# Performance work log

Hardware: AMD Instinct MI355X
Metric: run time of the kernel (lower is better)

## Reference

```python
import jax, jax.numpy as jnp
import numpy as np

N_HIDDEN = 2048
N_HEADS = 64
EXPAND = 2
D_STATE = 128
D_CONV = 4
CHUNK = 128
DT_MIN = 0.001
DT_MAX = 0.1
INNER = EXPAND * N_HIDDEN            # 4096
HEAD_DIM = INNER // N_HEADS          # 64
CONV_DIM = INNER + 2 * D_STATE       # 4352
D_IN_PROJ = 2 * INNER + 2 * D_STATE + N_HEADS  # 8512
EPS = 1e-6


def setup_inputs() -> dict:
    key = jax.random.key(0)
    ks = jax.random.split(key, 10)
    B, L = 2, 2048
    s = lambda fan_in: 1.0 / np.sqrt(fan_in)
    return {
        "x": jax.random.normal(ks[0], (B, L, N_HIDDEN), jnp.float32),
        "W_in": jax.random.normal(ks[1], (N_HIDDEN, D_IN_PROJ), jnp.float32) * s(N_HIDDEN),
        "b_in": jnp.zeros((D_IN_PROJ,), jnp.float32),
        "conv_w": jax.random.normal(ks[2], (D_CONV, 1, CONV_DIM), jnp.float32) * s(D_CONV),
        "conv_b": jnp.zeros((CONV_DIM,), jnp.float32),
        "A_log": jnp.log(jnp.arange(1, N_HEADS + 1, dtype=jnp.float32)),
        "dt_bias": jax.random.normal(ks[3], (N_HEADS,), jnp.float32) * 0.1,
        "D_param": jnp.ones((N_HEADS,), jnp.float32),
        "norm_w": jnp.ones((INNER,), jnp.float32),
        "W_out": jax.random.normal(ks[4], (INNER, N_HIDDEN), jnp.float32) * s(INNER),
        "b_out": jnp.zeros((N_HIDDEN,), jnp.float32),
    }


def _segsum(x):
    t = x.shape[-1]
    cs = jnp.cumsum(x, axis=-1)
    seg = cs[..., :, None] - cs[..., None, :]
    mask = jnp.tril(jnp.ones((t, t), dtype=bool))
    return jnp.where(mask, seg, -jnp.inf)


def _ssd(x, dt, a, b_mat, c_mat, d, dt_bias):
    # x: (B,L,H,P)  dt: (B,L,H)  a: (H,)  b_mat/c_mat: (B,L,H,N)  d: (H,)
    bsz, seq, h, p = x.shape
    dt = jnp.clip(jax.nn.softplus(dt + dt_bias), DT_MIN, DT_MAX)
    d_res = d.reshape(1, 1, h, 1) * x
    x_disc = x * dt[..., None]
    a_disc = a * dt                                   # (B,L,H)
    ch = lambda t_: t_.reshape(bsz, seq // CHUNK, CHUNK, *t_.shape[2:])
    x_blk, b_blk, c_blk = ch(x_disc), ch(b_mat), ch(c_mat)
    a_blk = jnp.transpose(ch(a_disc), (0, 3, 1, 2))   # (B,H,C,Lc)
    a_cum = jnp.cumsum(a_blk, axis=-1)
    l_mat = jnp.exp(_segsum(a_blk))                   # (B,H,C,Lc,Lc)
    y_diag = jnp.einsum("bclhn,bcshn,bhcls,bcshp->bclhp", c_blk, b_blk, l_mat, x_blk)
    decay_states = jnp.exp(a_cum[..., -1:] - a_cum)
    states = jnp.einsum("bclhn,bhcl,bclhp->bchpn", b_blk, decay_states, x_blk)
    states = jnp.concatenate([jnp.zeros_like(states[:, :1]), states], axis=1)
    a_end = jnp.pad(a_cum[..., -1], ((0, 0), (0, 0), (1, 0)))
    decay_chunk = jnp.exp(_segsum(a_end))
    new_states = jnp.einsum("bhzc,bchpn->bzhpn", decay_chunk, states)
    states = new_states[:, :-1]
    y_off = jnp.einsum("bclhn,bchpn,bhcl->bclhp", c_blk, states, jnp.exp(a_cum))
    y = (y_diag + y_off).reshape(bsz, seq, h, p)
    return y + d_res


def reference(x, W_in, b_in, conv_w, conv_b, A_log, dt_bias, D_param, norm_w, W_out, b_out):
    B, L, _ = x.shape
    zxbcdt = x @ W_in + b_in
    z = zxbcdt[..., :INNER]
    xBC = zxbcdt[..., INNER:INNER + CONV_DIM]
    dt = zxbcdt[..., -N_HEADS:]
    # causal depthwise conv1d + silu
    xp = jnp.pad(xBC, ((0, 0), (D_CONV - 1, 0), (0, 0)))
    xBC = jax.lax.conv_general_dilated(
        xp, conv_w, window_strides=(1,), padding="VALID",
        dimension_numbers=("NWC", "WIO", "NWC"), feature_group_count=CONV_DIM,
    ) + conv_b
    xBC = jax.nn.silu(xBC)
    x_ssm = xBC[..., :INNER].reshape(B, L, N_HEADS, HEAD_DIM)
    b_mat = jnp.broadcast_to(xBC[..., INNER:INNER + D_STATE][:, :, None, :], (B, L, N_HEADS, D_STATE))
    c_mat = jnp.broadcast_to(xBC[..., INNER + D_STATE:][:, :, None, :], (B, L, N_HEADS, D_STATE))
    a = -jnp.exp(A_log)
    y = _ssd(x_ssm, dt, a, b_mat, c_mat, D_param, dt_bias)
    y = y.reshape(B, L, INNER)
    # gated RMSNorm
    y = y * jax.nn.silu(z)
    y = y * jax.lax.rsqrt(jnp.mean(y * y, axis=-1, keepdims=True) + EPS) * norm_w
    return y @ W_out + b_out
```

## Files before the change

### kernel.cpp

```cpp
#include <hip/hip_runtime.h>
#include <hip/hip_bf16.h>
#include <cstdint>

typedef __bf16 bf16x8 __attribute__((ext_vector_type(8)));
typedef __bf16 bf16x4 __attribute__((ext_vector_type(4)));
typedef float  f4     __attribute__((ext_vector_type(4)));

constexpr int BATCH   = 2;
constexpr int LSEQ    = 2048;
constexpr int NH      = 2048;
constexpr int INNER   = 4096;
constexpr int DSTATE  = 128;
constexpr int CONVD   = 4352;
constexpr int HEADS   = 64;
constexpr int HDIM    = 64;
constexpr int NPROJ   = 8512;
constexpr int NPROJ_P = 8576;
constexpr int NC      = 16;
constexpr int CH      = 128;
constexpr int ROWS    = BATCH * LSEQ;
constexpr int NBC     = BATCH * NC;

__device__ __forceinline__ f4 f4zero() { f4 v; v.x=0.f; v.y=0.f; v.z=0.f; v.w=0.f; return v; }

__device__ __forceinline__ void gload16(const __bf16* g, __bf16* l) {
    __builtin_amdgcn_global_load_lds((const __attribute__((address_space(1))) void*)g,
                                     (__attribute__((address_space(3))) void*)l, 16, 0, 0);
}

__global__ __launch_bounds__(256) void k_cast_bf16(const float* __restrict__ in,
                                                   __bf16* __restrict__ out, int n4) {
    int i = blockIdx.x * 256 + threadIdx.x;
    if (i >= n4) return;
    f4 v = ((const f4*)in)[i];
    bf16x4 o;
    o[0] = (__bf16)v.x; o[1] = (__bf16)v.y; o[2] = (__bf16)v.z; o[3] = (__bf16)v.w;
    ((bf16x4*)out)[i] = o;
}

__global__ __launch_bounds__(256) void k_transpose_cast(const float* __restrict__ in,
                                                        __bf16* __restrict__ out,
                                                        int R, int C, int Cp) {
    __shared__ float tile[32][33];
    int bn = blockIdx.x * 32, bk = blockIdx.y * 32;
    int tx = threadIdx.x & 31, ty = threadIdx.x >> 5;
#pragma unroll
    for (int i = 0; i < 4; ++i) {
        int k = bk + ty + i * 8, n = bn + tx;
        tile[ty + i * 8][tx] = (k < R && n < C) ? in[(size_t)k * C + n] : 0.f;
    }
    __syncthreads();
#pragma unroll
    for (int i = 0; i < 4; ++i) {
        int n = bn + ty + i * 8, k = bk + tx;
        if (n < Cp && k < R) out[(size_t)n * R + k] = (__bf16)tile[tx][ty + i * 8];
    }
}

__global__ __launch_bounds__(256) void k_gemm1(const __bf16* __restrict__ A,
                                               const __bf16* __restrict__ Bt,
                                               const float* __restrict__ bias,
                                               __bf16* __restrict__ zf,
                                               __bf16* __restrict__ xbcpre,
                                               float* __restrict__ dtraw) {
    constexpr int K = NH;
    __shared__ __bf16 As[128 * 32];
    __shared__ __bf16 Bs[128 * 32];
    int tid = threadIdx.x;
    int lane = tid & 63, wave = tid >> 6;
    int wr = wave >> 1, wc = wave & 1;
    int mBase = blockIdx.y * 128, nBase = blockIdx.x * 128;
    int srow = lane >> 2, scol = (lane & 3) * 8;
    const __bf16* ga0 = A  + (size_t)(mBase + wave * 16 + srow) * K + scol;
    const __bf16* ga1 = ga0 + (size_t)64 * K;
    const __bf16* gb0 = Bt + (size_t)(nBase + wave * 16 + srow) * K + scol;
    const __bf16* gb1 = gb0 + (size_t)64 * K;
    __bf16* la0 = As + (wave * 16) * 32;
    __bf16* la1 = As + (64 + wave * 16) * 32;
    __bf16* lb0 = Bs + (wave * 16) * 32;
    __bf16* lb1 = Bs + (64 + wave * 16) * 32;
    f4 acc[4][4];
#pragma unroll
    for (int i = 0; i < 4; ++i)
#pragma unroll
        for (int j = 0; j < 4; ++j) acc[i][j] = f4zero();
    int kq = (lane >> 4) * 8, rl = lane & 15;
    for (int k0 = 0; k0 < K; k0 += 32) {
        __syncthreads();
        gload16(ga0 + k0, la0);
        gload16(ga1 + k0, la1);
        gload16(gb0 + k0, lb0);
        gload16(gb1 + k0, lb1);
        __syncthreads();
        bf16x8 af[4], bf[4];
#pragma unroll
        for (int i = 0; i < 4; ++i) {
            af[i] = *(const bf16x8*)&As[(wr * 64 + i * 16 + rl) * 32 + kq];
            bf[i] = *(const bf16x8*)&Bs[(wc * 64 + i * 16 + rl) * 32 + kq];
        }
#pragma unroll
        for (int mi = 0; mi < 4; ++mi)
#pragma unroll
            for (int ni = 0; ni < 4; ++ni)
                acc[mi][ni] = __builtin_amdgcn_mfma_f32_16x16x32_bf16(af[mi], bf[ni], acc[mi][ni], 0, 0, 0);
    }
    int rq = lane >> 4, cl = lane & 15;
#pragma unroll
    for (int ni = 0; ni < 4; ++ni) {
        int col0 = nBase + wc * 64 + ni * 16;
        int col = col0 + cl;
        if (col0 >= NPROJ) continue;
        float bv = bias[col];
#pragma unroll
        for (int mi = 0; mi < 4; ++mi) {
#pragma unroll
            for (int j = 0; j < 4; ++j) {
                int row = mBase + wr * 64 + mi * 16 + rq * 4 + j;
                float v = acc[mi][ni][j] + bv;
                if (col0 < INNER) {
                    zf[(size_t)row * INNER + col] = (__bf16)v;
                } else if (col0 < INNER + CONVD) {
                    xbcpre[(size_t)row * CONVD + (col - INNER)] = (__bf16)v;
                } else {
                    dtraw[(size_t)row * HEADS + (col - INNER - CONVD)] = v;
                }
            }
        }
    }
}

__global__ __launch_bounds__(256) void k_gemm_bf16(const __bf16* __restrict__ A,
                                                   const __bf16* __restrict__ Bt,
                                                   const float* __restrict__ bias,
                                                   float* __restrict__ C, int N, int K) {
    __shared__ __bf16 As[128 * 32];
    __shared__ __bf16 Bs[128 * 32];
    int tid = threadIdx.x;
    int lane = tid & 63, wave = tid >> 6;
    int wr = wave >> 1, wc = wave & 1;
    int mBase = blockIdx.y * 128, nBase = blockIdx.x * 128;
    int srow = lane >> 2, scol = (lane & 3) * 8;
    const __bf16* ga0 = A  + (size_t)(mBase + wave * 16 + srow) * K + scol;
    const __bf16* ga1 = ga0 + (size_t)64 * K;
    const __bf16* gb0 = Bt + (size_t)(nBase + wave * 16 + srow) * K + scol;
    const __bf16* gb1 = gb0 + (size_t)64 * K;
    __bf16* la0 = As + (wave * 16) * 32;
    __bf16* la1 = As + (64 + wave * 16) * 32;
    __bf16* lb0 = Bs + (wave * 16) * 32;
    __bf16* lb1 = Bs + (64 + wave * 16) * 32;
    f4 acc[4][4];
#pragma unroll
    for (int i = 0; i < 4; ++i)
#pragma unroll
        for (int j = 0; j < 4; ++j) acc[i][j] = f4zero();
    int kq = (lane >> 4) * 8, rl = lane & 15;
    for (int k0 = 0; k0 < K; k0 += 32) {
        __syncthreads();
        gload16(ga0 + k0, la0);
        gload16(ga1 + k0, la1);
        gload16(gb0 + k0, lb0);
        gload16(gb1 + k0, lb1);
        __syncthreads();
        bf16x8 af[4], bf[4];
#pragma unroll
        for (int i = 0; i < 4; ++i) {
            af[i] = *(const bf16x8*)&As[(wr * 64 + i * 16 + rl) * 32 + kq];
            bf[i] = *(const bf16x8*)&Bs[(wc * 64 + i * 16 + rl) * 32 + kq];
        }
#pragma unroll
        for (int mi = 0; mi < 4; ++mi)
#pragma unroll
            for (int ni = 0; ni < 4; ++ni)
                acc[mi][ni] = __builtin_amdgcn_mfma_f32_16x16x32_bf16(af[mi], bf[ni], acc[mi][ni], 0, 0, 0);
    }
    int rq = lane >> 4, cl = lane & 15;
#pragma unroll
    for (int ni = 0; ni < 4; ++ni) {
        int col = nBase + wc * 64 + ni * 16 + cl;
        float bv = bias[col];
#pragma unroll
        for (int mi = 0; mi < 4; ++mi)
#pragma unroll
            for (int j = 0; j < 4; ++j) {
                int row = mBase + wr * 64 + mi * 16 + rq * 4 + j;
                C[(size_t)row * N + col] = acc[mi][ni][j] + bv;
            }
    }
}

__global__ __launch_bounds__(256) void k_conv_silu(const __bf16* __restrict__ xbcpre,
                                                   const float* __restrict__ conv_w,
                                                   const float* __restrict__ conv_b,
                                                   __bf16* __restrict__ xbc) {
    int idx = blockIdx.x * 256 + threadIdx.x;
    int c8 = idx % (CONVD / 8);
    int bl = idx / (CONVD / 8);
    int l = bl & (LSEQ - 1);
    int c0 = c8 * 8;
    float acc[8];
    const f4* cb4 = (const f4*)(conv_b + c0);
    f4 b0 = cb4[0], b1 = cb4[1];
#pragma unroll
    for (int k = 0; k < 4; ++k) { acc[k] = b0[k]; acc[k + 4] = b1[k]; }
#pragma unroll
    for (int j = 0; j < 4; ++j) {
        int l2 = l + j - 3;
        if (l2 < 0) continue;
        bf16x8 xv = *(const bf16x8*)(xbcpre + (size_t)(bl + j - 3) * CONVD + c0);
        const f4* w4 = (const f4*)(conv_w + j * CONVD + c0);
        f4 w0 = w4[0], w1 = w4[1];
#pragma unroll
        for (int k = 0; k < 4; ++k) {
            acc[k]     += w0[k] * (float)xv[k];
            acc[k + 4] += w1[k] * (float)xv[k + 4];
        }
    }
    bf16x8 o;
#pragma unroll
    for (int k = 0; k < 8; ++k) {
        float a = acc[k];
        o[k] = (__bf16)(a / (1.f + expf(-a)));
    }
    *(bf16x8*)(xbc + (size_t)bl * CONVD + c0) = o;
}

__global__ __launch_bounds__(256) void k_dt(const float* __restrict__ dtraw,
                                            const float* __restrict__ dt_bias,
                                            float* __restrict__ dtp_t) {
    int idx = blockIdx.x * 256 + threadIdx.x;
    int h = idx & 63;
    int bl = idx >> 6;
    int b = bl >> 11, l = bl & (LSEQ - 1);
    float raw = dtraw[idx] + dt_bias[h];
    float sp = raw > 20.f ? raw : log1pf(expf(raw));
    dtp_t[((size_t)(b * HEADS + h)) * LSEQ + l] = fminf(fmaxf(sp, 0.001f), 0.1f);
}

__global__ __launch_bounds__(256) void k_transpose_bc(const __bf16* __restrict__ xbc,
                                                      __bf16* __restrict__ xT,
                                                      __bf16* __restrict__ BtG) {
    int bid = blockIdx.x;
    int ct = bid % 66;
    int rt = (bid / 66) & 1;
    int bc = bid / 132;
    __shared__ float T[64][65];
    int t = threadIdx.x;
    int lr0 = t >> 3, cg = t & 7;
#pragma unroll
    for (int it = 0; it < 2; ++it) {
        int lr = lr0 + it * 32;
        bf16x8 v = *(const bf16x8*)(xbc + (size_t)(bc * CH + rt * 64 + lr) * CONVD + ct * 64 + cg * 8);
#pragma unroll
        for (int j = 0; j < 8; ++j) T[lr][cg * 8 + j] = (float)v[j];
    }
    __syncthreads();
#pragma unroll
    for (int it = 0; it < 2; ++it) {
        int cl = lr0 + it * 32;
        int c = ct * 64 + cl;
        bf16x8 o;
#pragma unroll
        for (int j = 0; j < 8; ++j) o[j] = (__bf16)T[cg * 8 + j][cl];
        __bf16* dst = (c < INNER)
            ? xT  + ((size_t)bc * INNER + c) * CH + rt * 64 + cg * 8
            : BtG + ((size_t)bc * DSTATE + (c - INNER)) * CH + rt * 64 + cg * 8;
        *(bf16x8*)dst = o;
    }
}

__global__ __launch_bounds__(256) void k_cb(const __bf16* __restrict__ xbc,
                                            float* __restrict__ cbT) {
    int bid = blockIdx.x;
    int lg = bid & 7, bc = bid >> 3;
    int tid = threadIdx.x;
    int e0 = lg * 2048 + tid * 8;
    int l = e0 >> 7;
    int s0 = e0 & 127;
    const __bf16* Crow = xbc + (size_t)(bc * CH + l) * CONVD + INNER + DSTATE;
    const __bf16* B0   = xbc + (size_t)(bc * CH + s0) * CONVD + INNER;
    float acc[8];
#pragma unroll
    for (int j = 0; j < 8; ++j) acc[j] = 0.f;
    for (int n8 = 0; n8 < 16; ++n8) {
        bf16x8 cv = *(const bf16x8*)(Crow + n8 * 8);
        float cf[8];
#pragma unroll
        for (int k = 0; k < 8; ++k) cf[k] = (float)cv[k];
#pragma unroll
        for (int j = 0; j < 8; ++j) {
            bf16x8 bv = *(const bf16x8*)(B0 + (size_t)j * CONVD + n8 * 8);
#pragma unroll
            for (int k = 0; k < 8; ++k) acc[j] += cf[k] * (float)bv[k];
        }
    }
    float* dst = cbT + ((size_t)bc << 14) + (l << 7) + s0;
#pragma unroll
    for (int j = 0; j < 8; ++j) dst[j] = (s0 + j <= l) ? acc[j] : 0.f;
}

__global__ __launch_bounds__(256) void k_states(const __bf16* __restrict__ xT,
                                                const __bf16* __restrict__ BtG,
                                                const float* __restrict__ dtp_t,
                                                const float* __restrict__ A_log,
                                                __bf16* __restrict__ states,
                                                float* __restrict__ acum_buf,
                                                float* __restrict__ aend_buf) {
    int bid = blockIdx.x;
    int h = bid & 63, c = (bid >> 6) & 15, b = bid >> 10;
    int bc = b * NC + c, bh = b * HEADS + h;
    int tid = threadIdx.x;
    int lane = tid & 63, w = tid >> 6;
    __shared__ __bf16 Ab[64 * 136];
    __shared__ __bf16 Bb[128 * 136];
    __shared__ float s_ac[128], s_dt[128], s_e[128];
    float a_h = -expf(A_log[h]);

    if (tid < 128) {
        float d = dtp_t[(size_t)bh * LSEQ + c * CH + tid];
        s_dt[tid] = d;
        s_ac[tid] = a_h * d;
    }
    __syncthreads();
    for (int offd = 1; offd < 128; offd <<= 1) {
        float v = 0.f;
        if (tid < 128 && tid >= offd) v = s_ac[tid - offd];
        __syncthreads();
        if (tid < 128) s_ac[tid] += v;
        __syncthreads();
    }
    float aend = s_ac[127];
    if (tid < 128) {
        s_e[tid] = expf(aend - s_ac[tid]) * s_dt[tid];
        acum_buf[((size_t)bh * NC + c) * CH + tid] = s_ac[tid];
    }
    if (tid == 0) aend_buf[bh * NC + c] = aend;
    __syncthreads();

    const __bf16* xrow = xT + ((size_t)bc * INNER + h * HDIM) * CH;
#pragma unroll
    for (int it = 0; it < 4; ++it) {
        int task = it * 256 + tid;
        int p = task >> 4, lg2 = task & 15;
        bf16x8 v = *(const bf16x8*)(xrow + (size_t)p * CH + lg2 * 8);
        bf16x8 o;
#pragma unroll
        for (int j = 0; j < 8; ++j) o[j] = (__bf16)((float)v[j] * s_e[lg2 * 8 + j]);
        *(bf16x8*)&Ab[p * 136 + lg2 * 8] = o;
    }
    const __bf16* brow = BtG + (size_t)bc * DSTATE * CH;
#pragma unroll
    for (int it = 0; it < 8; ++it) {
        int task = it * 256 + tid;
        int n = task >> 4, lg2 = task & 15;
        *(bf16x8*)&Bb[n * 136 + lg2 * 8] = *(const bf16x8*)(brow + (size_t)n * CH + lg2 * 8);
    }
    __syncthreads();

    int rl = lane & 15, kq = (lane >> 4) * 8, rq = lane >> 4;
    f4 acc[8];
#pragma unroll
    for (int i = 0; i < 8; ++i) acc[i] = f4zero();
#pragma unroll
    for (int ks = 0; ks < 4; ++ks) {
        int k0 = ks * 32;
        bf16x8 a = *(const bf16x8*)&Ab[(w * 16 + rl) * 136 + k0 + kq];
#pragma unroll
        for (int nf = 0; nf < 8; ++nf) {
            bf16x8 bfr = *(const bf16x8*)&Bb[(nf * 16 + rl) * 136 + k0 + kq];
            acc[nf] = __builtin_amdgcn_mfma_f32_16x16x32_bf16(a, bfr, acc[nf], 0, 0, 0);
        }
    }
    __syncthreads();
#pragma unroll
    for (int nf = 0; nf < 8; ++nf)
#pragma unroll
        for (int j = 0; j < 4; ++j)
            Ab[(w * 16 + rq * 4 + j) * 136 + nf * 16 + rl] = (__bf16)acc[nf][j];
    __syncthreads();
    __bf16* sbase = states + ((size_t)(bc * HEADS + h)) * (HDIM * DSTATE);
#pragma unroll
    for (int it = 0; it < 4; ++it) {
        int task = it * 256 + tid;
        int p = task >> 4, ng = task & 15;
        *(bf16x8*)(sbase + (size_t)p * DSTATE + ng * 8) = *(const bf16x8*)&Ab[p * 136 + ng * 8];
    }
}

__global__ __launch_bounds__(256) void k_scan(__bf16* __restrict__ states,
                                              const float* __restrict__ aend_buf) {
    int bh = blockIdx.x;
    int b = bh >> 6, h = bh & 63;
    int tid = threadIdx.x;
    float run[4][8];
#pragma unroll
    for (int i = 0; i < 4; ++i)
#pragma unroll
        for (int j = 0; j < 8; ++j) run[i][j] = 0.f;
    for (int c = 0; c < NC; ++c) {
        float dec = expf(aend_buf[bh * NC + c]);
        bf16x8* base = (bf16x8*)(states + ((size_t)((b * NC + c) * HEADS + h)) * (HDIM * DSTATE));
#pragma unroll
        for (int i = 0; i < 4; ++i) {
            bf16x8 s = base[i * 256 + tid];
            bf16x8 o;
#pragma unroll
            for (int j = 0; j < 8; ++j) o[j] = (__bf16)run[i][j];
            base[i * 256 + tid] = o;
#pragma unroll
            for (int j = 0; j < 8; ++j) run[i][j] = run[i][j] * dec + (float)s[j];
        }
    }
}

__global__ __launch_bounds__(256) void k_out(const __bf16* __restrict__ xbc,
                                             const __bf16* __restrict__ xT,
                                             const float* __restrict__ dtp_t,
                                             const float* __restrict__ cbT,
                                             const __bf16* __restrict__ prev,
                                             const float* __restrict__ acum_buf,
                                             const float* __restrict__ D_param,
                                             __bf16* __restrict__ ybuf) {
    int bid = blockIdx.x;
    int h = bid & 63, c = (bid >> 6) & 15, b = bid >> 10;
    int bc = b * NC + c, bh = b * HEADS + h;
    int tid = threadIdx.x;
    int lane = tid & 63, w = tid >> 6;
    __shared__ __bf16 Ab[128 * 136];
    __shared__ __bf16 Bb[64 * 136];
    __shared__ float s_ac[128], s_dt[128];
    if (tid < 128) {
        s_ac[tid] = acum_buf[((size_t)bh * NC + c) * CH + tid];
        s_dt[tid] = dtp_t[(size_t)bh * LSEQ + c * CH + tid];
    }

#pragma unroll
    for (int it = 0; it < 8; ++it) {
        int task = it * 256 + tid;
        int l = task >> 4, ng = task & 15;
        *(bf16x8*)&Ab[l * 136 + ng * 8] =
            *(const bf16x8*)(xbc + (size_t)(bc * CH + l) * CONVD + INNER + DSTATE + ng * 8);
    }
    const __bf16* pbase = prev + ((size_t)(bc * HEADS + h)) * (HDIM * DSTATE);
#pragma unroll
    for (int it = 0; it < 4; ++it) {
        int task = it * 256 + tid;
        int p = task >> 4, ng = task & 15;
        *(bf16x8*)&Bb[p * 136 + ng * 8] = *(const bf16x8*)(pbase + (size_t)p * DSTATE + ng * 8);
    }
    __syncthreads();

    int rl = lane & 15, kq = (lane >> 4) * 8, rq = lane >> 4;
    f4 acc[2][4];
#pragma unroll
    for (int i = 0; i < 2; ++i)
#pragma unroll
        for (int j = 0; j < 4; ++j) acc[i][j] = f4zero();

#pragma unroll
    for (int ks = 0; ks < 4; ++ks) {
        int k0 = ks * 32;
        bf16x8 a0 = *(const bf16x8*)&Ab[(w * 32 + rl) * 136 + k0 + kq];
        bf16x8 a1 = *(const bf16x8*)&Ab[(w * 32 + 16 + rl) * 136 + k0 + kq];
#pragma unroll
        for (int nf = 0; nf < 4; ++nf) {
            bf16x8 bfr = *(const bf16x8*)&Bb[(nf * 16 + rl) * 136 + k0 + kq];
            acc[0][nf] = __builtin_amdgcn_mfma_f32_16x16x32_bf16(a0, bfr, acc[0][nf], 0, 0, 0);
            acc[1][nf] = __builtin_amdgcn_mfma_f32_16x16x32_bf16(a1, bfr, acc[1][nf], 0, 0, 0);
        }
    }
#pragma unroll
    for (int mf = 0; mf < 2; ++mf)
#pragma unroll
        for (int j = 0; j < 4; ++j) {
            float el = expf(s_ac[w * 32 + mf * 16 + rq * 4 + j]);
#pragma unroll
            for (int nf = 0; nf < 4; ++nf) acc[mf][nf][j] *= el;
        }
    __syncthreads();

    const float* cbb = cbT + ((size_t)bc << 14);
#pragma unroll
    for (int it = 0; it < 8; ++it) {
        int task = it * 256 + tid;
        int l = task >> 4, sg = task & 15;
        int s0 = sg * 8;
        const f4* cv4 = (const f4*)(cbb + (l << 7) + s0);
        f4 c0 = cv4[0], c1 = cv4[1];
        float acl = s_ac[l];
        bf16x8 o;
#pragma unroll
        for (int j = 0; j < 8; ++j) {
            int s = s0 + j;
            float cj = (j < 4) ? c0[j] : c1[j - 4];
            float m = 0.f;
            if (s <= l) m = cj * expf(acl - s_ac[s]) * s_dt[s];
            o[j] = (__bf16)m;
        }
        *(bf16x8*)&Ab[l * 136 + s0] = o;
    }
    const __bf16* xrow = xT + ((size_t)bc * INNER + h * HDIM) * CH;
#pragma unroll
    for (int it = 0; it < 4; ++it) {
        int task = it * 256 + tid;
        int p = task >> 4, lg2 = task & 15;
        *(bf16x8*)&Bb[p * 136 + lg2 * 8] = *(const bf16x8*)(xrow + (size_t)p * CH + lg2 * 8);
    }
    __syncthreads();

#pragma unroll
    for (int ks = 0; ks < 4; ++ks) {
        int k0 = ks * 32;
        bf16x8 a0 = *(const bf16x8*)&Ab[(w * 32 + rl) * 136 + k0 + kq];
        bf16x8 a1 = *(const bf16x8*)&Ab[(w * 32 + 16 + rl) * 136 + k0 + kq];
#pragma unroll
        for (int nf = 0; nf < 4; ++nf) {
            bf16x8 bfr = *(const bf16x8*)&Bb[(nf * 16 + rl) * 136 + k0 + kq];
            acc[0][nf] = __builtin_amdgcn_mfma_f32_16x16x32_bf16(a0, bfr, acc[0][nf], 0, 0, 0);
            acc[1][nf] = __builtin_amdgcn_mfma_f32_16x16x32_bf16(a1, bfr, acc[1][nf], 0, 0, 0);
        }
    }
    __syncthreads();

    float* yT = (float*)Ab;
#pragma unroll
    for (int mf = 0; mf < 2; ++mf)
#pragma unroll
        for (int nf = 0; nf < 4; ++nf)
#pragma unroll
            for (int j = 0; j < 4; ++j)
                yT[(w * 32 + mf * 16 + rq * 4 + j) * 68 + nf * 16 + rl] = acc[mf][nf][j];
    __syncthreads();

    float dh = D_param[h];
#pragma unroll
    for (int it = 0; it < 4; ++it) {
        int task = it * 256 + tid;
        int l = task >> 3, pg = task & 7;
        const f4* yv4 = (const f4*)&yT[l * 68 + pg * 8];
        f4 y0 = yv4[0], y1 = yv4[1];
        bf16x8 xv = *(const bf16x8*)(xbc + (size_t)(bc * CH + l) * CONVD + h * HDIM + pg * 8);
        bf16x8 o;
#pragma unroll
        for (int j = 0; j < 4; ++j) {
            o[j]     = (__bf16)(y0[j] + dh * (float)xv[j]);
            o[j + 4] = (__bf16)(y1[j] + dh * (float)xv[j + 4]);
        }
        *(bf16x8*)(ybuf + (size_t)(bc * CH + l) * INNER + h * HDIM + pg * 8) = o;
    }
}

__global__ __launch_bounds__(256) void k_gate_norm(__bf16* __restrict__ ybuf,
                                                   const __bf16* __restrict__ zf,
                                                   const float* __restrict__ norm_w) {
    int row = blockIdx.x, tid = threadIdx.x;
    bf16x8* yrow = (bf16x8*)(ybuf + (size_t)row * INNER);
    const bf16x8* zrow = (const bf16x8*)(zf + (size_t)row * INNER);
    float v[2][8];
    float ss = 0.f;
#pragma unroll
    for (int i = 0; i < 2; ++i) {
        bf16x8 yv = yrow[i * 256 + tid];
        bf16x8 zv = zrow[i * 256 + tid];
#pragma unroll
        for (int j = 0; j < 8; ++j) {
            float z = (float)zv[j];
            float t = (float)yv[j] * (z / (1.f + expf(-z)));
            v[i][j] = t;
            ss += t * t;
        }
    }
#pragma unroll
    for (int off = 32; off > 0; off >>= 1) ss += __shfl_down(ss, off, 64);
    __shared__ float red[4];
    __shared__ float scs;
    if ((tid & 63) == 0) red[tid >> 6] = ss;
    __syncthreads();
    if (tid == 0) scs = rsqrtf((red[0] + red[1] + red[2] + red[3]) * (1.f / INNER) + 1e-6f);
    __syncthreads();
    float scale = scs;
#pragma unroll
    for (int i = 0; i < 2; ++i) {
        const f4* nw = (const f4*)(norm_w + (i * 256 + tid) * 8);
        f4 w0 = nw[0], w1 = nw[1];
        bf16x8 o;
#pragma unroll
        for (int j = 0; j < 4; ++j) {
            o[j]     = (__bf16)(v[i][j]     * scale * w0[j]);
            o[j + 4] = (__bf16)(v[i][j + 4] * scale * w1[j]);
        }
        yrow[i * 256 + tid] = o;
    }
}

extern "C" void kernel_launch(void* const* d_in, const int* in_sizes, int n_in,
                              void* d_out, int out_size, void* d_ws, size_t ws_size,
                              hipStream_t stream) {
    const float* x       = (const float*)d_in[0];
    const float* W_in    = (const float*)d_in[1];
    const float* b_in    = (const float*)d_in[2];
    const float* conv_w  = (const float*)d_in[3];
    const float* conv_b  = (const float*)d_in[4];
    const float* A_log   = (const float*)d_in[5];
    const float* dt_bias = (const float*)d_in[6];
    const float* D_par   = (const float*)d_in[7];
    const float* norm_w  = (const float*)d_in[8];
    const float* W_out   = (const float*)d_in[9];
    const float* b_out   = (const float*)d_in[10];
    float* out = (float*)d_out;

    char* ws = (char*)d_ws;
    constexpr size_t SZ_XBF    = (size_t)ROWS * NH * 2;
    constexpr size_t SZ_WTIN   = (size_t)NPROJ_P * NH * 2;
    constexpr size_t SZ_R1     = SZ_XBF + SZ_WTIN;
    constexpr size_t SZ_ZF     = (size_t)ROWS * INNER * 2;
    constexpr size_t SZ_XBC    = (size_t)ROWS * CONVD * 2;
    constexpr size_t SZ_STATES = (size_t)NBC * HEADS * HDIM * DSTATE * 2;
    constexpr size_t SZ_CBT    = (size_t)NBC * CH * CH * 4;
    constexpr size_t SZ_ACUM   = (size_t)BATCH * HEADS * NC * CH * 4;
    constexpr size_t SZ_AEND   = (size_t)BATCH * HEADS * NC * 4;
    constexpr size_t SZ_DTP    = (size_t)ROWS * HEADS * 4;

    __bf16* xbf    = (__bf16*)(ws);
    __bf16* wtin   = (__bf16*)(ws + SZ_XBF);
    __bf16* zf     = (__bf16*)(ws + SZ_R1);
    __bf16* xbcpre = (__bf16*)(ws + SZ_R1 + SZ_ZF);
    __bf16* xbc    = (__bf16*)(ws + SZ_R1 + SZ_ZF + SZ_XBC);
    float*  dtraw  = (float*) (ws + SZ_R1 + SZ_ZF + 2 * SZ_XBC);
    __bf16* states = (__bf16*)(ws);
    float*  cbT    = (float*) (ws + SZ_STATES);
    float*  acum   = (float*) (ws + SZ_STATES + SZ_CBT);
    float*  aend   = (float*) (ws + SZ_STATES + SZ_CBT + SZ_ACUM);
    float*  dtp_t  = (float*) (ws + SZ_STATES + SZ_CBT + SZ_ACUM + SZ_AEND);
    __bf16* BtG    = (__bf16*)(ws + SZ_STATES + SZ_CBT + SZ_ACUM + SZ_AEND + SZ_DTP);
    __bf16* ybuf   = xbcpre;
    __bf16* wtout  = xbc;
    __bf16* xT     = (__bf16*)out;

    (void)ws_size; (void)in_sizes; (void)n_in; (void)out_size;

    k_cast_bf16<<<(ROWS * NH / 4 + 255) / 256, 256, 0, stream>>>(x, xbf, ROWS * NH / 4);
    k_transpose_cast<<<dim3(NPROJ_P / 32, NH / 32), 256, 0, stream>>>(W_in, wtin, NH, NPROJ, NPROJ_P);

    k_gemm1<<<dim3(NPROJ_P / 128, ROWS / 128), 256, 0, stream>>>(xbf, wtin, b_in, zf, xbcpre, dtraw);

    k_conv_silu<<<ROWS * (CONVD / 8) / 256, 256, 0, stream>>>(xbcpre, conv_w, conv_b, xbc);
    k_dt<<<ROWS * HEADS / 256, 256, 0, stream>>>(dtraw, dt_bias, dtp_t);
    k_transpose_bc<<<NBC * 132, 256, 0, stream>>>(xbc, xT, BtG);
    k_cb<<<NBC * 8, 256, 0, stream>>>(xbc, cbT);
    k_states<<<NBC * HEADS, 256, 0, stream>>>(xT, BtG, dtp_t, A_log, states, acum, aend);
    k_scan<<<BATCH * HEADS, 256, 0, stream>>>(states, aend);
    k_out<<<NBC * HEADS, 256, 0, stream>>>(xbc, xT, dtp_t, cbT, states, acum, D_par, ybuf);
    k_gate_norm<<<ROWS, 256, 0, stream>>>(ybuf, zf, norm_w);

    k_transpose_cast<<<dim3(NH / 32, INNER / 32), 256, 0, stream>>>(W_out, wtout, INNER, NH, NH);
    k_gemm_bf16<<<dim3(NH / 128, ROWS / 128), 256, 0, stream>>>(ybuf, wtout, b_out, out, NH, INNER);
}
```

Measured before the change: 513.6 us.

## Replace GEMMs with double-buffered 256-tile 8-wave kernel and split scan across blocks

Both projection GEMMs move to a templated 512-thread kernel with 256x256 or 256x128 tiles, 64-wide K steps and double-buffered LDS loads via global_load_lds. It also uses swizzled LDS reads, interleaved prefetch inside the MFMA loop, setprio hints and XCD-aware block remapping. The point is to cut LDS and global-load stalls and barrier overhead relative to the single-buffered 128x128 kernel. The chunk-state scan also splits each (batch, head) across 8 blocks of 128 threads for more parallelism. NPROJ_P padding grows so the 256-wide tiles divide it, which adds some wasted compute and a large dynamic LDS footprint.

```diff
diff --git a/kernel.cpp b/kernel.cpp
--- a/kernel.cpp
+++ b/kernel.cpp
@@ -15,7 +15,7 @@
 constexpr int HEADS   = 64;
 constexpr int HDIM    = 64;
 constexpr int NPROJ   = 8512;
-constexpr int NPROJ_P = 8576;
+constexpr int NPROJ_P = 8704;
 constexpr int NC      = 16;
 constexpr int CH      = 128;
 constexpr int ROWS    = BATCH * LSEQ;
@@ -23,7 +23,7 @@
 
 __device__ __forceinline__ f4 f4zero() { f4 v; v.x=0.f; v.y=0.f; v.z=0.f; v.w=0.f; return v; }
 
-__device__ __forceinline__ void gload16(const __bf16* g, __bf16* l) {
+__device__ __forceinline__ void gload16(const __bf16* g, const char* l) {
     __builtin_amdgcn_global_load_lds((const __attribute__((address_space(1))) void*)g,
                                      (__attribute__((address_space(3))) void*)l, 16, 0, 0);
 }
@@ -57,134 +57,152 @@
     }
 }
 
-__global__ __launch_bounds__(256) void k_gemm1(const __bf16* __restrict__ A,
-                                               const __bf16* __restrict__ Bt,
-                                               const float* __restrict__ bias,
-                                               __bf16* __restrict__ zf,
-                                               __bf16* __restrict__ xbcpre,
-                                               float* __restrict__ dtraw) {
-    constexpr int K = NH;
-    __shared__ __bf16 As[128 * 32];
-    __shared__ __bf16 Bs[128 * 32];
-    int tid = threadIdx.x;
-    int lane = tid & 63, wave = tid >> 6;
-    int wr = wave >> 1, wc = wave & 1;
-    int mBase = blockIdx.y * 128, nBase = blockIdx.x * 128;
-    int srow = lane >> 2, scol = (lane & 3) * 8;
-    const __bf16* ga0 = A  + (size_t)(mBase + wave * 16 + srow) * K + scol;
-    const __bf16* ga1 = ga0 + (size_t)64 * K;
-    const __bf16* gb0 = Bt + (size_t)(nBase + wave * 16 + srow) * K + scol;
-    const __bf16* gb1 = gb0 + (size_t)64 * K;
-    __bf16* la0 = As + (wave * 16) * 32;
-    __bf16* la1 = As + (64 + wave * 16) * 32;
-    __bf16* lb0 = Bs + (wave * 16) * 32;
-    __bf16* lb1 = Bs + (64 + wave * 16) * 32;
-    f4 acc[4][4];
-#pragma unroll
-    for (int i = 0; i < 4; ++i)
-#pragma unroll
-        for (int j = 0; j < 4; ++j) acc[i][j] = f4zero();
-    int kq = (lane >> 4) * 8, rl = lane & 15;
-    for (int k0 = 0; k0 < K; k0 += 32) {
-        __syncthreads();
-        gload16(ga0 + k0, la0);
-        gload16(ga1 + k0, la1);
-        gload16(gb0 + k0, lb0);
-        gload16(gb1 + k0, lb1);
-        __syncthreads();
-        bf16x8 af[4], bf[4];
-#pragma unroll
-        for (int i = 0; i < 4; ++i) {
-            af[i] = *(const bf16x8*)&As[(wr * 64 + i * 16 + rl) * 32 + kq];
-            bf[i] = *(const bf16x8*)&Bs[(wc * 64 + i * 16 + rl) * 32 + kq];
-        }
-#pragma unroll
-        for (int mi = 0; mi < 4; ++mi)
-#pragma unroll
-            for (int ni = 0; ni < 4; ++ni)
-                acc[mi][ni] = __builtin_amdgcn_mfma_f32_16x16x32_bf16(af[mi], bf[ni], acc[mi][ni], 0, 0, 0);
-    }
-    int rq = lane >> 4, cl = lane & 15;
-#pragma unroll
-    for (int ni = 0; ni < 4; ++ni) {
-        int col0 = nBase + wc * 64 + ni * 16;
+template<int BM, int BN, int WM, int WN, int EPI>
+__global__ __launch_bounds__(512, 2) void k_gemm8(
+    const __bf16* __restrict__ A, const __bf16* __restrict__ Bt,
+    const float* __restrict__ bias, float* __restrict__ Cf,
+    __bf16* __restrict__ zf, __bf16* __restrict__ xbcpre, float* __restrict__ dtraw,
+    int N, int K, int gridX) {
+    extern __shared__ char smem[];
+    constexpr int MFRAG = BM / (WM * 16);
+    constexpr int NFRAG = BN / (WN * 16);
+    constexpr int MH = MFRAG / 2, NH2 = NFRAG / 2;
+    constexpr int ALINES = BM / 64, BLINES = BN / 64, LT = ALINES + BLINES;
+    constexpr int ABYTES = BM * 128, BUFB = ABYTES + BN * 128;
+    constexpr int LPPA = BM / 128, LPPB = BN / 128;
+
+    int tid = threadIdx.x, lane = tid & 63, w = tid >> 6;
+    int wm = w / WN, wn = w % WN;
+
+    int bid = blockIdx.x;
+    int q = gridDim.x >> 3;
+    int wg = (bid & 7) * q + (bid >> 3);
+    int by = wg / gridX, bx = wg - by * gridX;
+    int mBase = by * BM, nBase = bx * BN;
+
+    int rl = lane & 15, rq = lane >> 4;
+    int kslp = rq ^ (((rl >> 3) & 1) << 1);
+    const int rdA = (wm * MFRAG * 16 + rl) * 64 + kslp * 16;
+    const int rdB = ABYTES + (wn * NFRAG * 16 + rl) * 64 + kslp * 16;
+
+    int lanep = lane ^ (((lane >> 5) & 1) << 1);
+    int srs = lanep >> 2, sksl = lanep & 3;
+
+    const __bf16* sA[ALINES];
+#pragma unroll
+    for (int li = 0; li < ALINES; ++li)
+        sA[li] = A + (size_t)(mBase + (li % LPPA) * 128 + w * 16 + srs) * K + (li / LPPA) * 32 + sksl * 8;
+    const __bf16* sB[BLINES];
+#pragma unroll
+    for (int li = 0; li < BLINES; ++li)
+        sB[li] = Bt + (size_t)(nBase + (li % LPPB) * 128 + w * 16 + srs) * K + (li / LPPB) * 32 + sksl * 8;
+
+    auto stage = [&](int buf, int line, int kt) {
+        if (line < ALINES) {
+            gload16(sA[line] + kt, smem + buf * BUFB + line * 8192 + w * 1024);
+        } else {
+            int lb = line - ALINES;
+            gload16(sB[lb] + kt, smem + buf * BUFB + ABYTES + lb * 8192 + w * 1024);
+        }
+    };
+
+    f4 acc[MFRAG][NFRAG];
+#pragma unroll
+    for (int i = 0; i < MFRAG; ++i)
+#pragma unroll
+        for (int j = 0; j < NFRAG; ++j) acc[i][j] = f4zero();
+
+    const int nt = K >> 6;
+#pragma unroll
+    for (int li = 0; li < LT; ++li) stage(0, li, 0);
+    stage(1, 0, 64);
+    stage(1, 1, 64);
+    asm volatile("s_waitcnt vmcnt(2)" ::: "memory");
+    __builtin_amdgcn_s_barrier();
+
+    for (int t = 0; t < nt; ++t) {
+        const int cur = t & 1;
+        const int bufoff = cur * BUFB;
+        const bool hasNext = (t + 1 < nt);
+        const int ktn = (t + 1) << 6;
+#pragma unroll
+        for (int p = 0; p < 4; ++p) {
+            const int mh = p >> 1, nh = p & 1;
+            bf16x8 af[MH][2], bv[NH2][2];
+#pragma unroll
+            for (int mi = 0; mi < MH; ++mi)
+#pragma unroll
+                for (int ks = 0; ks < 2; ++ks)
+                    af[mi][ks] = *(const bf16x8*)(smem + bufoff + ks * (BM * 64) + rdA + (mh * MH + mi) * 1024);
+#pragma unroll
+            for (int ni = 0; ni < NH2; ++ni)
+#pragma unroll
+                for (int ks = 0; ks < 2; ++ks)
+                    bv[ni][ks] = *(const bf16x8*)(smem + bufoff + ks * (BN * 64) + rdB + (nh * NH2 + ni) * 1024);
+            if (hasNext) {
+                if (2 + 2 * p < LT) stage(cur ^ 1, 2 + 2 * p, ktn);
+                if (3 + 2 * p < LT) stage(cur ^ 1, 3 + 2 * p, ktn);
+            }
+            __builtin_amdgcn_s_barrier();
+            asm volatile("s_waitcnt lgkmcnt(0)" ::: "memory");
+            __builtin_amdgcn_sched_barrier(0);
+            __builtin_amdgcn_s_setprio(1);
+#pragma unroll
+            for (int mi = 0; mi < MH; ++mi)
+#pragma unroll
+                for (int ni = 0; ni < NH2; ++ni)
+#pragma unroll
+                    for (int ks = 0; ks < 2; ++ks)
+                        acc[mh * MH + mi][nh * NH2 + ni] =
+                            __builtin_amdgcn_mfma_f32_16x16x32_bf16(af[mi][ks], bv[ni][ks],
+                                                                    acc[mh * MH + mi][nh * NH2 + ni], 0, 0, 0);
+            __builtin_amdgcn_s_setprio(0);
+            __builtin_amdgcn_s_barrier();
+        }
+        if (t + 2 < nt) {
+            stage(cur, 0, (t + 2) << 6);
+            stage(cur, 1, (t + 2) << 6);
+            asm volatile("s_waitcnt vmcnt(2)" ::: "memory");
+            __builtin_amdgcn_s_barrier();
+        } else if (hasNext) {
+            asm volatile("s_waitcnt vmcnt(0)" ::: "memory");
+            __builtin_amdgcn_s_barrier();
+        }
+    }
+
+    int cl = lane & 15, rq4 = (lane >> 4) * 4;
+#pragma unroll
+    for (int nf = 0; nf < NFRAG; ++nf) {
+        int col0 = nBase + wn * NFRAG * 16 + nf * 16;
         int col = col0 + cl;
-        if (col0 >= NPROJ) continue;
-        float bv = bias[col];
-#pragma unroll
-        for (int mi = 0; mi < 4; ++mi) {
-#pragma unroll
-            for (int j = 0; j < 4; ++j) {
-                int row = mBase + wr * 64 + mi * 16 + rq * 4 + j;
-                float v = acc[mi][ni][j] + bv;
-                if (col0 < INNER) {
-                    zf[(size_t)row * INNER + col] = (__bf16)v;
-                } else if (col0 < INNER + CONVD) {
-                    xbcpre[(size_t)row * CONVD + (col - INNER)] = (__bf16)v;
-                } else {
-                    dtraw[(size_t)row * HEADS + (col - INNER - CONVD)] = v;
+        if constexpr (EPI == 1) {
+            if (col0 >= NPROJ) continue;
+            float bvv = bias[col];
+#pragma unroll
+            for (int mf = 0; mf < MFRAG; ++mf) {
+#pragma unroll
+                for (int j = 0; j < 4; ++j) {
+                    int row = mBase + wm * MFRAG * 16 + mf * 16 + rq4 + j;
+                    float v = acc[mf][nf][j] + bvv;
+                    if (col0 < INNER) {
+                        zf[(size_t)row * INNER + col] = (__bf16)v;
+                    } else if (col0 < INNER + CONVD) {
+                        xbcpre[(size_t)row * CONVD + (col - INNER)] = (__bf16)v;
+                    } else {
+                        dtraw[(size_t)row * HEADS + (col - INNER - CONVD)] = v;
+                    }
                 }
             }
-        }
-    }
-}
-
-__global__ __launch_bounds__(256) void k_gemm_bf16(const __bf16* __restrict__ A,
-                                                   const __bf16* __restrict__ Bt,
-                                                   const float* __restrict__ bias,
-                                                   float* __restrict__ C, int N, int K) {
-    __shared__ __bf16 As[128 * 32];
-    __shared__ __bf16 Bs[128 * 32];
-    int tid = threadIdx.x;
-    int lane = tid & 63, wave = tid >> 6;
-    int wr = wave >> 1, wc = wave & 1;
-    int mBase = blockIdx.y * 128, nBase = blockIdx.x * 128;
-    int srow = lane >> 2, scol = (lane & 3) * 8;
-    const __bf16* ga0 = A  + (size_t)(mBase + wave * 16 + srow) * K + scol;
-    const __bf16* ga1 = ga0 + (size_t)64 * K;
-    const __bf16* gb0 = Bt + (size_t)(nBase + wave * 16 + srow) * K + scol;
-    const __bf16* gb1 = gb0 + (size_t)64 * K;
-    __bf16* la0 = As + (wave * 16) * 32;
-    __bf16* la1 = As + (64 + wave * 16) * 32;
-    __bf16* lb0 = Bs + (wave * 16) * 32;
-    __bf16* lb1 = Bs + (64 + wave * 16) * 32;
-    f4 acc[4][4];
-#pragma unroll
-    for (int i = 0; i < 4; ++i)
-#pragma unroll
-        for (int j = 0; j < 4; ++j) acc[i][j] = f4zero();
-    int kq = (lane >> 4) * 8, rl = lane & 15;
-    for (int k0 = 0; k0 < K; k0 += 32) {
-        __syncthreads();
-        gload16(ga0 + k0, la0);
-        gload16(ga1 + k0, la1);
-        gload16(gb0 + k0, lb0);
-        gload16(gb1 + k0, lb1);
-        __syncthreads();
-        bf16x8 af[4], bf[4];
-#pragma unroll
-        for (int i = 0; i < 4; ++i) {
-            af[i] = *(const bf16x8*)&As[(wr * 64 + i * 16 + rl) * 32 + kq];
-            bf[i] = *(const bf16x8*)&Bs[(wc * 64 + i * 16 + rl) * 32 + kq];
-        }
-#pragma unroll
-        for (int mi = 0; mi < 4; ++mi)
-#pragma unroll
-            for (int ni = 0; ni < 4; ++ni)
-                acc[mi][ni] = __builtin_amdgcn_mfma_f32_16x16x32_bf16(af[mi], bf[ni], acc[mi][ni], 0, 0, 0);
-    }
-    int rq = lane >> 4, cl = lane & 15;
-#pragma unroll
-    for (int ni = 0; ni < 4; ++ni) {
-        int col = nBase + wc * 64 + ni * 16 + cl;
-        float bv = bias[col];
-#pragma unroll
-        for (int mi = 0; mi < 4; ++mi)
-#pragma unroll
-            for (int j = 0; j < 4; ++j) {
-                int row = mBase + wr * 64 + mi * 16 + rq * 4 + j;
-                C[(size_t)row * N + col] = acc[mi][ni][j] + bv;
-            }
+        } else {
+            float bvv = bias[col];
+#pragma unroll
+            for (int mf = 0; mf < MFRAG; ++mf)
+#pragma unroll
+                for (int j = 0; j < 4; ++j) {
+                    int row = mBase + wm * MFRAG * 16 + mf * 16 + rq4 + j;
+                    Cf[(size_t)row * N + col] = acc[mf][nf][j] + bvv;
+                }
+        }
     }
 }
 
@@ -288,9 +306,9 @@
         for (int k = 0; k < 8; ++k) cf[k] = (float)cv[k];
 #pragma unroll
         for (int j = 0; j < 8; ++j) {
-            bf16x8 bv = *(const bf16x8*)(B0 + (size_t)j * CONVD + n8 * 8);
-#pragma unroll
-            for (int k = 0; k < 8; ++k) acc[j] += cf[k] * (float)bv[k];
+            bf16x8 bvv = *(const bf16x8*)(B0 + (size_t)j * CONVD + n8 * 8);
+#pragma unroll
+            for (int k = 0; k < 8; ++k) acc[j] += cf[k] * (float)bvv[k];
         }
     }
     float* dst = cbT + ((size_t)bc << 14) + (l << 7) + s0;
@@ -386,29 +404,26 @@
     }
 }
 
-__global__ __launch_bounds__(256) void k_scan(__bf16* __restrict__ states,
+__global__ __launch_bounds__(128) void k_scan(__bf16* __restrict__ states,
                                               const float* __restrict__ aend_buf) {
-    int bh = blockIdx.x;
+    int s = blockIdx.x & 7;
+    int bh = blockIdx.x >> 3;
     int b = bh >> 6, h = bh & 63;
     int tid = threadIdx.x;
-    float run[4][8];
-#pragma unroll
-    for (int i = 0; i < 4; ++i)
-#pragma unroll
-        for (int j = 0; j < 8; ++j) run[i][j] = 0.f;
+    size_t off = (size_t)s * 1024 + (size_t)tid * 8;
+    float run[8];
+#pragma unroll
+    for (int j = 0; j < 8; ++j) run[j] = 0.f;
     for (int c = 0; c < NC; ++c) {
         float dec = expf(aend_buf[bh * NC + c]);
-        bf16x8* base = (bf16x8*)(states + ((size_t)((b * NC + c) * HEADS + h)) * (HDIM * DSTATE));
-#pragma unroll
-        for (int i = 0; i < 4; ++i) {
-            bf16x8 s = base[i * 256 + tid];
-            bf16x8 o;
-#pragma unroll
-            for (int j = 0; j < 8; ++j) o[j] = (__bf16)run[i][j];
-            base[i * 256 + tid] = o;
-#pragma unroll
-            for (int j = 0; j < 8; ++j) run[i][j] = run[i][j] * dec + (float)s[j];
-        }
+        __bf16* base = states + ((size_t)((b * NC + c) * HEADS + h)) * (HDIM * DSTATE) + off;
+        bf16x8 sv = *(bf16x8*)base;
+        bf16x8 o;
+#pragma unroll
+        for (int j = 0; j < 8; ++j) o[j] = (__bf16)run[j];
+        *(bf16x8*)base = o;
+#pragma unroll
+        for (int j = 0; j < 8; ++j) run[j] = run[j] * dec + (float)sv[j];
     }
 }
 
@@ -638,20 +653,27 @@
 
     (void)ws_size; (void)in_sizes; (void)n_in; (void)out_size;
 
+    hipFuncSetAttribute(reinterpret_cast<const void*>(&k_gemm8<256,256,2,4,1>),
+                        hipFuncAttributeMaxDynamicSharedMemorySize, 131072);
+    hipFuncSetAttribute(reinterpret_cast<const void*>(&k_gemm8<256,128,4,2,0>),
+                        hipFuncAttributeMaxDynamicSharedMemorySize, 98304);
+
     k_cast_bf16<<<(ROWS * NH / 4 + 255) / 256, 256, 0, stream>>>(x, xbf, ROWS * NH / 4);
     k_transpose_cast<<<dim3(NPROJ_P / 32, NH / 32), 256, 0, stream>>>(W_in, wtin, NH, NPROJ, NPROJ_P);
 
-    k_gemm1<<<dim3(NPROJ_P / 128, ROWS / 128), 256, 0, stream>>>(xbf, wtin, b_in, zf, xbcpre, dtraw);
+    k_gemm8<256,256,2,4,1><<<(NPROJ_P / 256) * (ROWS / 256), 512, 131072, stream>>>(
+        xbf, wtin, b_in, nullptr, zf, xbcpre, dtraw, NPROJ_P, NH, NPROJ_P / 256);
 
     k_conv_silu<<<ROWS * (CONVD / 8) / 256, 256, 0, stream>>>(xbcpre, conv_w, conv_b, xbc);
     k_dt<<<ROWS * HEADS / 256, 256, 0, stream>>>(dtraw, dt_bias, dtp_t);
     k_transpose_bc<<<NBC * 132, 256, 0, stream>>>(xbc, xT, BtG);
     k_cb<<<NBC * 8, 256, 0, stream>>>(xbc, cbT);
     k_states<<<NBC * HEADS, 256, 0, stream>>>(xT, BtG, dtp_t, A_log, states, acum, aend);
-    k_scan<<<BATCH * HEADS, 256, 0, stream>>>(states, aend);
+    k_scan<<<BATCH * HEADS * 8, 128, 0, stream>>>(states, aend);
     k_out<<<NBC * HEADS, 256, 0, stream>>>(xbc, xT, dtp_t, cbT, states, acum, D_par, ybuf);
     k_gate_norm<<<ROWS, 256, 0, stream>>>(ybuf, zf, norm_w);
 
     k_transpose_cast<<<dim3(NH / 32, INNER / 32), 256, 0, stream>>>(W_out, wtout, INNER, NH, NH);
-    k_gemm_bf16<<<dim3(NH / 128, ROWS / 128), 256, 0, stream>>>(ybuf, wtout, b_out, out, NH, INNER);
-}
+    k_gemm8<256,128,4,2,0><<<(NH / 128) * (ROWS / 256), 512, 98304, stream>>>(
+        ybuf, wtout, b_out, out, nullptr, nullptr, nullptr, NH, INNER, NH / 128);
+}
```

After: 516.0 us. About the same (+0.5%).
